# Kernel tuning notes

Hardware: AMD Instinct MI355X
Metric: run time of the kernel (lower is better)

Reference implementation:

```python
import jax, jax.numpy as jnp
import numpy as np


def _lstm_step(x, h, c, Wih, Whh, bih, bhh):
    # PyTorch LSTMCell gate order: i, f, g, o
    g = x @ Wih.T + bih + h @ Whh.T + bhh
    i, f, gg, o = jnp.split(g, 4, axis=1)
    c = jax.nn.sigmoid(f) * c + jax.nn.sigmoid(i) * jnp.tanh(gg)
    h = jax.nn.sigmoid(o) * jnp.tanh(c)
    return h, c


def _canvas2seq(canvas):
    # Valid objects (row-sum >= 0) compacted to the front, rest padded with -1.
    mask = canvas.sum(axis=2) >= 0                       # [B, 25]
    order = jnp.argsort(jnp.where(mask, 0, 1), axis=1, stable=True)
    gathered = jnp.take_along_axis(canvas, order[:, :, None], axis=1)
    smask = jnp.take_along_axis(mask, order, axis=1)
    return jnp.where(smask[:, :, None], gathered, jnp.float32(-1.0))


def _canvas_encode(canvas, Wobj, bobj, ce_Wih, ce_Whh, ce_bih, ce_bhh):
    seq = _canvas2seq(canvas)                            # [B, 25, 4]
    x = seq @ Wobj.T + bobj                              # [B, 25, 64]
    B = x.shape[0]
    h = jnp.zeros((B, 64), x.dtype)
    c = jnp.zeros((B, 64), x.dtype)

    def step(carry, xt):
        h, c = carry
        h, c = _lstm_step(xt, h, c, ce_Wih, ce_Whh, ce_bih, ce_bhh)
        return (h, c), None

    (h, _), _ = jax.lax.scan(step, (h, c), jnp.swapaxes(x, 0, 1))
    return h


def setup_inputs() -> dict:
    key = jax.random.key(0)
    ks = jax.random.split(key, 16)
    B, T, V = 256, 65, 10000
    IN, H = 64, 128
    s = 0.05
    inp = {}
    inp["inst"] = jax.random.randint(ks[0], (B, T), 0, V)
    inp["prev_canvas"] = jax.random.uniform(ks[1], (B, 25, 4), dtype=jnp.float32)
    inp["final_canvas"] = jax.random.uniform(ks[2], (B, 25, 4), dtype=jnp.float32)
    inp["target_obj"] = jax.random.normal(ks[3], (B, 4), dtype=jnp.float32)
    inp["embed_W"] = jax.random.normal(ks[4], (V + 1, IN), dtype=jnp.float32) * s
    inp["Wih"] = jax.random.normal(ks[5], (4 * H, IN), dtype=jnp.float32) * s
    inp["Whh"] = jax.random.normal(ks[6], (4 * H, H), dtype=jnp.float32) * s
    inp["bih"] = jnp.zeros((4 * H,), jnp.float32)
    inp["bhh"] = jnp.zeros((4 * H,), jnp.float32)
    inp["Wout"] = jax.random.normal(ks[7], (V + 1, H), dtype=jnp.float32) * s
    inp["bout"] = jnp.zeros((V + 1,), jnp.float32)
    inp["Wtgt"] = jax.random.normal(ks[8], (IN, 4), dtype=jnp.float32) * s
    inp["btgt"] = jnp.zeros((IN,), jnp.float32)
    inp["Wobj"] = jax.random.normal(ks[9], (64, 4), dtype=jnp.float32) * s
    inp["bobj"] = jnp.zeros((64,), jnp.float32)
    inp["ce_Wih"] = jax.random.normal(ks[10], (256, 64), dtype=jnp.float32) * s
    inp["ce_Whh"] = jax.random.normal(ks[11], (256, 64), dtype=jnp.float32) * s
    inp["ce_bih"] = jnp.zeros((256,), jnp.float32)
    inp["ce_bhh"] = jnp.zeros((256,), jnp.float32)
    return inp


def reference(inst, prev_canvas, final_canvas, target_obj,
              embed_W, Wih, Whh, bih, bhh, Wout, bout,
              Wtgt, btgt, Wobj, bobj, ce_Wih, ce_Whh, ce_bih, ce_bhh):
    B, H = inst.shape[0], 128
    tgt_emb = target_obj @ Wtgt.T + btgt                 # [B, 64]
    enc = (_canvas_encode(prev_canvas, Wobj, bobj, ce_Wih, ce_Whh, ce_bih, ce_bhh)
           + _canvas_encode(final_canvas, Wobj, bobj, ce_Wih, ce_Whh, ce_bih, ce_bhh))
    h = jnp.zeros((B, H), jnp.float32)
    c = jnp.zeros((B, H), jnp.float32)
    h, c = _lstm_step(enc, h, c, Wih, Whh, bih, bhh)
    h, c = _lstm_step(tgt_emb, h, c, Wih, Whh, bih, bhh)

    tokens = inst[:, :-1].T                              # [T-1, B]

    def step(carry, it):
        h, c = carry
        xt = embed_W[it]                                 # [B, 64]
        h, c = _lstm_step(xt, h, c, Wih, Whh, bih, bhh)
        lp = jax.nn.log_softmax(h @ Wout.T + bout, axis=1)
        return (h, c), lp

    _, lps = jax.lax.scan(step, (h, c), tokens)          # [T-1, B, V+1]
    return jnp.swapaxes(lps, 0, 1)                       # [B, T-1, V+1]
```

## Files before the change

kernel.cpp:

```cpp
#include <hip/hip_runtime.h>
#include <stdint.h>

typedef __attribute__((ext_vector_type(4))) float f32x4;
typedef __attribute__((ext_vector_type(8))) short s16x8;
typedef __attribute__((ext_vector_type(8))) unsigned short us8;

__device__ __forceinline__ float bf2f(unsigned short u){
  union { unsigned int i; float f; } v; v.i = ((unsigned int)u) << 16; return v.f;
}
__device__ __forceinline__ unsigned short f2bf(float f){
  union { float f; unsigned int i; } v; v.f = f;
  unsigned int r = v.i + 0x7FFFu + ((v.i >> 16) & 1u);
  return (unsigned short)(r >> 16);
}
__device__ __forceinline__ float sigm(float x){ return 1.0f / (1.0f + __expf(-x)); }

#define NA (10240*128)
#define NB 10240
#define ND 512
#define NE (256*64)
#define NF 32768

__global__ void k_prep(const float* __restrict__ Wout, const float* __restrict__ bout,
                       const float* __restrict__ bih,  const float* __restrict__ bhh,
                       const float* __restrict__ tobj, const float* __restrict__ Wtgt,
                       const float* __restrict__ btgt,
                       const float* __restrict__ ceWih, const float* __restrict__ ceWhh,
                       unsigned short* __restrict__ WoutP, float* __restrict__ boutP,
                       float* __restrict__ bsum, float* __restrict__ tgt,
                       unsigned short* __restrict__ cePack)
{
  int tid = blockIdx.x * 256 + threadIdx.x;
  if (tid < NA){
    int vv = tid >> 7, k = tid & 127;
    float val = (vv < 10001) ? Wout[vv*128 + k] : 0.0f;
    WoutP[tid] = f2bf(val);
  } else if (tid < NA+NB){
    int vv = tid - NA;
    boutP[vv] = (vv < 10001) ? bout[vv] : -1e30f;
  } else if (tid < NA+NB+ND){
    int g = tid - NA - NB;
    bsum[g] = bih[g] + bhh[g];
  } else if (tid < NA+NB+ND+NE){
    int i = tid - NA - NB - ND; int b = i >> 6, j = i & 63;
    const float* to = tobj + b*4; const float* wt = Wtgt + j*4;
    tgt[i] = btgt[j] + to[0]*wt[0] + to[1]*wt[1] + to[2]*wt[2] + to[3]*wt[3];
  } else if (tid < NA+NB+ND+NE+NF){
    int i = tid - NA - NB - ND - NE;
    int half = i >> 14;
    int r = (i >> 6) & 255;
    int k = i & 63;
    int k8 = k >> 3;
    int slot = ((k8 ^ (r & 7)) << 3) | (k & 7);
    const float* src = half ? ceWhh : ceWih;
    cePack[half*16384 + r*64 + slot] = f2bf(src[r*64 + k]);
  }
}

__global__ __launch_bounds__(256) void k_canvas(
    const float* __restrict__ prevC, const float* __restrict__ finC,
    const float* __restrict__ Wobj,  const float* __restrict__ bobj,
    const unsigned short* __restrict__ cePack,
    const float* __restrict__ cebih, const float* __restrict__ cebhh,
    float* __restrict__ encP, float* __restrict__ encF)
{
  __shared__ unsigned short wih[256*64] __attribute__((aligned(16)));
  __shared__ unsigned short whh[256*64] __attribute__((aligned(16)));
  __shared__ float seq[25*4];
  __shared__ float xb[64] __attribute__((aligned(16)));
  __shared__ float hb[2][64] __attribute__((aligned(16)));
  __shared__ float gates[256];
  __shared__ float wobj_s[256];
  __shared__ float bobj_s[64];
  __shared__ float bsum_ce[256];

  int tid = threadIdx.x;
  int b = blockIdx.x & 255;
  int which = blockIdx.x >> 8;
  const float* canvas = (which ? finC : prevC) + b*100;

  {
    const us8* cp = (const us8*)cePack;
    us8* wl = (us8*)wih;
    us8* hl = (us8*)whh;
    for (int i = tid; i < 2048; i += 256){
      wl[i] = cp[i];
      hl[i] = cp[2048 + i];
    }
  }
  wobj_s[tid] = Wobj[tid];
  if (tid < 64) bobj_s[tid] = bobj[tid];
  bsum_ce[tid] = cebih[tid] + cebhh[tid];
  if (tid < 64) hb[0][tid] = 0.0f;
  if (tid == 0){
    int pos = 0;
    for (int i = 0; i < 25; i++){
      float a0=canvas[i*4+0], a1=canvas[i*4+1], a2=canvas[i*4+2], a3=canvas[i*4+3];
      if (a0+a1+a2+a3 >= 0.0f){
        seq[pos*4+0]=a0; seq[pos*4+1]=a1; seq[pos*4+2]=a2; seq[pos*4+3]=a3; pos++;
      }
    }
    for (; pos < 25; pos++){
      seq[pos*4+0]=-1.0f; seq[pos*4+1]=-1.0f; seq[pos*4+2]=-1.0f; seq[pos*4+3]=-1.0f;
    }
  }
  __syncthreads();

  float creg = 0.0f;
  int cur = 0;
  const float4* x4 = (const float4*)xb;

  for (int t = 0; t < 25; t++){
    if (tid < 64){
      float a = bobj_s[tid];
      a += wobj_s[tid*4+0]*seq[t*4+0] + wobj_s[tid*4+1]*seq[t*4+1]
         + wobj_s[tid*4+2]*seq[t*4+2] + wobj_s[tid*4+3]*seq[t*4+3];
      xb[tid] = a;
    }
    __syncthreads();
    float acc = bsum_ce[tid];
    const float4* h4 = (const float4*)hb[cur];
    int rowoff = tid*64;
    int sw = tid & 7;
    #pragma unroll
    for (int k8 = 0; k8 < 8; k8++){
      int slot = ((k8 ^ sw) * 8);
      us8 w1 = *reinterpret_cast<const us8*>(&wih[rowoff + slot]);
      us8 w2 = *reinterpret_cast<const us8*>(&whh[rowoff + slot]);
      float4 xa = x4[2*k8], xc = x4[2*k8+1];
      float4 ha = h4[2*k8], hc = h4[2*k8+1];
      acc += bf2f(w1[0])*xa.x + bf2f(w1[1])*xa.y + bf2f(w1[2])*xa.z + bf2f(w1[3])*xa.w;
      acc += bf2f(w1[4])*xc.x + bf2f(w1[5])*xc.y + bf2f(w1[6])*xc.z + bf2f(w1[7])*xc.w;
      acc += bf2f(w2[0])*ha.x + bf2f(w2[1])*ha.y + bf2f(w2[2])*ha.z + bf2f(w2[3])*ha.w;
      acc += bf2f(w2[4])*hc.x + bf2f(w2[5])*hc.y + bf2f(w2[6])*hc.z + bf2f(w2[7])*hc.w;
    }
    gates[tid] = acc;
    __syncthreads();
    if (tid < 64){
      float i_ = sigm(gates[tid]);
      float f_ = sigm(gates[64+tid]);
      float g_ = tanhf(gates[128+tid]);
      float o_ = sigm(gates[192+tid]);
      creg = f_*creg + i_*g_;
      hb[cur^1][tid] = o_ * tanhf(creg);
    }
    __syncthreads();
    cur ^= 1;
  }
  if (tid < 64){
    (which ? encF : encP)[b*64 + tid] = hb[cur][tid];
  }
}

__global__ __launch_bounds__(512, 2) void k_rec(
    const float* __restrict__ Whh, const float* __restrict__ Wih,
    const float* __restrict__ bsum, const int* __restrict__ inst,
    const float* __restrict__ embW, const float* __restrict__ tgt,
    const float* __restrict__ encP, const float* __restrict__ encF,
    unsigned short* __restrict__ Hout)
{
  int b = blockIdx.x;
  int g = threadIdx.x;
  __shared__ float xb[2][64] __attribute__((aligned(16)));
  __shared__ float hb[2][128] __attribute__((aligned(16)));
  __shared__ float gates[512];

  float wreg[128];
  float ureg[64];
  {
    const float4* wrow = (const float4*)(Whh + g*128);
    #pragma unroll
    for (int k4 = 0; k4 < 32; k4++){
      float4 w = wrow[k4];
      wreg[4*k4+0]=w.x; wreg[4*k4+1]=w.y; wreg[4*k4+2]=w.z; wreg[4*k4+3]=w.w;
    }
    const float4* urow = (const float4*)(Wih + g*64);
    #pragma unroll
    for (int k4 = 0; k4 < 16; k4++){
      float4 w = urow[k4];
      ureg[4*k4+0]=w.x; ureg[4*k4+1]=w.y; ureg[4*k4+2]=w.z; ureg[4*k4+3]=w.w;
    }
  }
  float bz = bsum[g];
  float creg = 0.0f;
  if (g < 128) hb[0][g] = 0.0f;
  if (g < 64)  xb[0][g] = encP[b*64+g] + encF[b*64+g];
  int cur = 0;
  __syncthreads();

  for (int s = 0; s < 66; s++){
    float a0 = bz, a1 = 0.0f, a2 = 0.0f, a3 = 0.0f;
    const float4* h4 = (const float4*)hb[cur];
    const float4* x4 = (const float4*)xb[cur];
    #pragma unroll
    for (int k4 = 0; k4 < 32; k4 += 4){
      float4 h0 = h4[k4], h1 = h4[k4+1], h2 = h4[k4+2], h3 = h4[k4+3];
      a0 += wreg[4*k4+0]*h0.x + wreg[4*k4+1]*h0.y + wreg[4*k4+2]*h0.z + wreg[4*k4+3]*h0.w;
      a1 += wreg[4*k4+4]*h1.x + wreg[4*k4+5]*h1.y + wreg[4*k4+6]*h1.z + wreg[4*k4+7]*h1.w;
      a2 += wreg[4*k4+8]*h2.x + wreg[4*k4+9]*h2.y + wreg[4*k4+10]*h2.z + wreg[4*k4+11]*h2.w;
      a3 += wreg[4*k4+12]*h3.x + wreg[4*k4+13]*h3.y + wreg[4*k4+14]*h3.z + wreg[4*k4+15]*h3.w;
    }
    #pragma unroll
    for (int k4 = 0; k4 < 16; k4 += 4){
      float4 x0 = x4[k4], x1 = x4[k4+1], x2 = x4[k4+2], x3 = x4[k4+3];
      a0 += ureg[4*k4+0]*x0.x + ureg[4*k4+1]*x0.y + ureg[4*k4+2]*x0.z + ureg[4*k4+3]*x0.w;
      a1 += ureg[4*k4+4]*x1.x + ureg[4*k4+5]*x1.y + ureg[4*k4+6]*x1.z + ureg[4*k4+7]*x1.w;
      a2 += ureg[4*k4+8]*x2.x + ureg[4*k4+9]*x2.y + ureg[4*k4+10]*x2.z + ureg[4*k4+11]*x2.w;
      a3 += ureg[4*k4+12]*x3.x + ureg[4*k4+13]*x3.y + ureg[4*k4+14]*x3.z + ureg[4*k4+15]*x3.w;
    }
    gates[g] = (a0 + a1) + (a2 + a3);
    __syncthreads();
    if (g < 128){
      float i_ = sigm(gates[g]);
      float f_ = sigm(gates[128+g]);
      float g_ = tanhf(gates[256+g]);
      float o_ = sigm(gates[384+g]);
      creg = f_*creg + i_*g_;
      float h = o_ * tanhf(creg);
      hb[cur^1][g] = h;
      if (s >= 2) Hout[((size_t)(b*64 + (s-2)))*128 + g] = f2bf(h);
    } else if (g < 192 && s < 65){
      int l = g - 128;
      float v;
      if (s + 1 == 1) v = tgt[b*64 + l];
      else { int tok = inst[b*65 + (s - 1)]; v = embW[tok*64 + l]; }
      xb[cur^1][l] = v;
    }
    __syncthreads();
    cur ^= 1;
  }
}

__global__ __launch_bounds__(512, 4) void k_out(
    const unsigned short* __restrict__ Hout, const unsigned short* __restrict__ WoutP,
    const float* __restrict__ boutP, float* __restrict__ out)
{
  extern __shared__ float stage[];
  __shared__ float rs_l[8][32];
  __shared__ float lse_l[32];

  int blk = blockIdx.x;
  int r0 = blk * 32;
  int tid = threadIdx.x;
  int w = tid >> 6;
  int l = tid & 63;
  int lm = l & 15;
  int lq = l >> 4;
  int kof = lq * 8;
  size_t obase = (size_t)r0 * 10001u;

  s16x8 af[2][4];
  #pragma unroll
  for (int c = 0; c < 2; c++){
    const s16x8* ap = (const s16x8*)(Hout + (size_t)(r0 + c*16 + lm)*128 + kof);
    #pragma unroll
    for (int kk = 0; kk < 4; kk++) af[c][kk] = ap[kk*4];
  }

  s16x8 b0[4], b1[4], b2[4];
#define LOADB(dst, tl) { \
    const s16x8* bp_ = (const s16x8*)(WoutP + (size_t)((tl)*16 + lm)*128 + kof); \
    dst[0] = bp_[0]; dst[1] = bp_[4]; dst[2] = bp_[8]; dst[3] = bp_[12]; }

  float rs[2][4] = {};
#define P1C(buf, tl) { \
    f32x4 a0_ = {0,0,0,0}, a1_ = {0,0,0,0}; \
    _Pragma("unroll") \
    for (int kk = 0; kk < 4; kk++){ \
      a0_ = __builtin_amdgcn_mfma_f32_16x16x32_bf16(af[0][kk], buf[kk], a0_, 0, 0, 0); \
      a1_ = __builtin_amdgcn_mfma_f32_16x16x32_bf16(af[1][kk], buf[kk], a1_, 0, 0, 0); } \
    float bo_ = boutP[(tl)*16 + lm]; \
    _Pragma("unroll") \
    for (int i = 0; i < 4; i++){ rs[0][i] += __expf(a0_[i] + bo_); rs[1][i] += __expf(a1_[i] + bo_); } }

  {
    int tl = w;
    LOADB(b0, tl); LOADB(b1, tl + 8);
    for (int p = 0; p < 26; p++){
      LOADB(b2, tl + 16); P1C(b0, tl);
      LOADB(b0, tl + 24); P1C(b1, tl + 8);
      LOADB(b1, tl + 32); P1C(b2, tl + 16);
      tl += 24;
    }
    P1C(b0, tl);
    P1C(b1, tl + 8);
  }

  #pragma unroll
  for (int c = 0; c < 2; c++){
    #pragma unroll
    for (int i = 0; i < 4; i++){
      float s = rs[c][i];
      s += __shfl_xor(s, 1); s += __shfl_xor(s, 2);
      s += __shfl_xor(s, 4); s += __shfl_xor(s, 8);
      rs[c][i] = s;
    }
  }
  if (lm == 0){
    #pragma unroll
    for (int c = 0; c < 2; c++)
      #pragma unroll
      for (int i = 0; i < 4; i++)
        rs_l[w][c*16 + lq*4 + i] = rs[c][i];
  }

#define T2(c,q) ((c)*32 + w*4 + (q))
  LOADB(b0, T2(0,0)); LOADB(b1, T2(0,1));

#define BAR() { asm volatile("s_waitcnt lgkmcnt(0)" ::: "memory"); __builtin_amdgcn_s_barrier(); }

  BAR();
  if (tid < 32){
    float s = rs_l[0][tid] + rs_l[1][tid] + rs_l[2][tid] + rs_l[3][tid]
            + rs_l[4][tid] + rs_l[5][tid] + rs_l[6][tid] + rs_l[7][tid];
    lse_l[tid] = logf(s);
  }
  BAR();
  float ml[2][4];
  #pragma unroll
  for (int c = 0; c < 2; c++)
    #pragma unroll
    for (int i = 0; i < 4; i++)
      ml[c][i] = lse_l[c*16 + lq*4 + i];

#define P2C(buf, tl, q) { \
    f32x4 a0_ = {0,0,0,0}, a1_ = {0,0,0,0}; \
    _Pragma("unroll") \
    for (int kk = 0; kk < 4; kk++){ \
      a0_ = __builtin_amdgcn_mfma_f32_16x16x32_bf16(af[0][kk], buf[kk], a0_, 0, 0, 0); \
      a1_ = __builtin_amdgcn_mfma_f32_16x16x32_bf16(af[1][kk], buf[kk], a1_, 0, 0, 0); } \
    float bo_ = boutP[(tl)*16 + lm]; \
    int colq_ = (w*4 + (q))*16 + lm; \
    _Pragma("unroll") \
    for (int i = 0; i < 4; i++){ \
      stage[(0*16 + lq*4 + i)*516 + colq_] = a0_[i] + bo_ - ml[0][i]; \
      stage[(1*16 + lq*4 + i)*516 + colq_] = a1_[i] + bo_ - ml[1][i]; } }

#define WPHASE(c) { \
    int vbase_ = (c)*512; \
    if ((c) < 19){ \
      _Pragma("unroll 4") \
      for (int j = 0; j < 32; j++){ \
        int e_ = j*512 + tid; int row_ = e_ >> 9; int cc_ = e_ & 511; \
        __builtin_nontemporal_store(stage[row_*516 + cc_], \
            &out[obase + (size_t)row_*10001u + (unsigned)(vbase_ + cc_)]); } \
    } else { \
      _Pragma("unroll 4") \
      for (int j = 0; j < 32; j++){ \
        int e_ = j*512 + tid; int row_ = e_ >> 9; int cc_ = e_ & 511; \
        if (vbase_ + cc_ < 10001) \
          __builtin_nontemporal_store(stage[row_*516 + cc_], \
              &out[obase + (size_t)row_*10001u + (unsigned)(vbase_ + cc_)]); } } }

#define CHUNK(ba,bb,bc,c) { \
    LOADB(bc, T2(c,2));     P2C(ba, T2(c,0), 0); \
    LOADB(ba, T2(c,3));     P2C(bb, T2(c,1), 1); \
    LOADB(bb, T2((c)+1,0)); P2C(bc, T2(c,2), 2); \
    LOADB(bc, T2((c)+1,1)); P2C(ba, T2(c,3), 3); \
    BAR(); WPHASE(c); BAR(); }

  for (int cb = 0; cb < 18; cb += 3){
    CHUNK(b0, b1, b2, cb);
    CHUNK(b1, b2, b0, cb + 1);
    CHUNK(b2, b0, b1, cb + 2);
  }
  CHUNK(b0, b1, b2, 18);
  LOADB(b0, T2(19,2)); P2C(b1, T2(19,0), 0);
  LOADB(b1, T2(19,3)); P2C(b2, T2(19,1), 1);
  P2C(b0, T2(19,2), 2);
  P2C(b1, T2(19,3), 3);
  BAR();
  WPHASE(19);
}

extern "C" void kernel_launch(void* const* d_in, const int* in_sizes, int n_in,
                              void* d_out, int out_size, void* d_ws, size_t ws_size,
                              hipStream_t stream)
{
  (void)in_sizes; (void)n_in; (void)out_size; (void)ws_size;
  const int*   inst    = (const int*)  d_in[0];
  const float* prevC   = (const float*)d_in[1];
  const float* finC    = (const float*)d_in[2];
  const float* tobj    = (const float*)d_in[3];
  const float* embW    = (const float*)d_in[4];
  const float* Wih     = (const float*)d_in[5];
  const float* Whh     = (const float*)d_in[6];
  const float* bih     = (const float*)d_in[7];
  const float* bhh     = (const float*)d_in[8];
  const float* Wout    = (const float*)d_in[9];
  const float* bout    = (const float*)d_in[10];
  const float* Wtgt    = (const float*)d_in[11];
  const float* btgt    = (const float*)d_in[12];
  const float* Wobj    = (const float*)d_in[13];
  const float* bobj    = (const float*)d_in[14];
  const float* ceWih   = (const float*)d_in[15];
  const float* ceWhh   = (const float*)d_in[16];
  const float* cebih   = (const float*)d_in[17];
  const float* cebhh   = (const float*)d_in[18];

  char* ws = (char*)d_ws;
  unsigned short* WoutP = (unsigned short*)(ws + 0);
  float* boutP = (float*)(ws + 2621440);
  float* bsum  = (float*)(ws + 2662400);
  float* tgt   = (float*)(ws + 2664448);
  float* encP  = (float*)(ws + 2729984);
  float* encF  = (float*)(ws + 2795520);
  unsigned short* Hout = (unsigned short*)(ws + 2861056);
  unsigned short* cePack = (unsigned short*)(ws + 7055360);
  float* out = (float*)d_out;

  hipFuncSetAttribute((const void*)k_out,
                      hipFuncAttributeMaxDynamicSharedMemorySize, 66048);

  k_prep  <<<5354, 256, 0, stream>>>(Wout, bout, bih, bhh, tobj, Wtgt, btgt,
                                     ceWih, ceWhh, WoutP, boutP, bsum, tgt, cePack);
  k_canvas<<<512, 256, 0, stream>>>(prevC, finC, Wobj, bobj, cePack,
                                    cebih, cebhh, encP, encF);
  k_rec   <<<256, 512, 0, stream>>>(Whh, Wih, bsum, inst, embW, tgt, encP, encF, Hout);
  k_out   <<<512, 512, 66048, stream>>>(Hout, WoutP, boutP, out);
}
```

Baseline: 561.6 us.

## Halve rows per block in output projection to raise occupancy

The logits/log-softmax kernel now processes 16 rows per block instead of 32, launches 1024 blocks, and uses static 33KB shared staging with launch bounds allowing 8 waves per SIMD. Register buffers shrink (one A fragment set, double instead of triple B buffering). This aims to improve latency hiding and spread the store-bound work across more resident blocks. In exchange, each block re-reads the full Wout matrix, so Wout traffic doubles and MFMA reuse of each B fragment halves.

```diff
diff --git a/kernel.cpp b/kernel.cpp
--- a/kernel.cpp
+++ b/kernel.cpp
@@ -231,16 +231,16 @@
   }
 }
 
-__global__ __launch_bounds__(512, 4) void k_out(
+__global__ __launch_bounds__(512, 8) void k_out(
     const unsigned short* __restrict__ Hout, const unsigned short* __restrict__ WoutP,
     const float* __restrict__ boutP, float* __restrict__ out)
 {
-  extern __shared__ float stage[];
-  __shared__ float rs_l[8][32];
-  __shared__ float lse_l[32];
+  __shared__ float stage[16*516];
+  __shared__ float rs_l[8][16];
+  __shared__ float lse_l[16];
 
   int blk = blockIdx.x;
-  int r0 = blk * 32;
+  int r0 = blk * 16;
   int tid = threadIdx.x;
   int w = tid >> 6;
   int l = tid & 63;
@@ -249,128 +249,106 @@
   int kof = lq * 8;
   size_t obase = (size_t)r0 * 10001u;
 
-  s16x8 af[2][4];
-  #pragma unroll
-  for (int c = 0; c < 2; c++){
-    const s16x8* ap = (const s16x8*)(Hout + (size_t)(r0 + c*16 + lm)*128 + kof);
-    #pragma unroll
-    for (int kk = 0; kk < 4; kk++) af[c][kk] = ap[kk*4];
-  }
-
-  s16x8 b0[4], b1[4], b2[4];
+  s16x8 af[4];
+  {
+    const s16x8* ap = (const s16x8*)(Hout + (size_t)(r0 + lm)*128 + kof);
+    #pragma unroll
+    for (int kk = 0; kk < 4; kk++) af[kk] = ap[kk*4];
+  }
+
+  s16x8 b0[4], b1[4];
 #define LOADB(dst, tl) { \
     const s16x8* bp_ = (const s16x8*)(WoutP + (size_t)((tl)*16 + lm)*128 + kof); \
     dst[0] = bp_[0]; dst[1] = bp_[4]; dst[2] = bp_[8]; dst[3] = bp_[12]; }
 
-  float rs[2][4] = {};
+  float rs[4] = {0,0,0,0};
 #define P1C(buf, tl) { \
-    f32x4 a0_ = {0,0,0,0}, a1_ = {0,0,0,0}; \
+    f32x4 a_ = {0,0,0,0}; \
     _Pragma("unroll") \
-    for (int kk = 0; kk < 4; kk++){ \
-      a0_ = __builtin_amdgcn_mfma_f32_16x16x32_bf16(af[0][kk], buf[kk], a0_, 0, 0, 0); \
-      a1_ = __builtin_amdgcn_mfma_f32_16x16x32_bf16(af[1][kk], buf[kk], a1_, 0, 0, 0); } \
+    for (int kk = 0; kk < 4; kk++) \
+      a_ = __builtin_amdgcn_mfma_f32_16x16x32_bf16(af[kk], buf[kk], a_, 0, 0, 0); \
     float bo_ = boutP[(tl)*16 + lm]; \
     _Pragma("unroll") \
-    for (int i = 0; i < 4; i++){ rs[0][i] += __expf(a0_[i] + bo_); rs[1][i] += __expf(a1_[i] + bo_); } }
+    for (int i = 0; i < 4; i++) rs[i] += __expf(a_[i] + bo_); }
 
   {
     int tl = w;
-    LOADB(b0, tl); LOADB(b1, tl + 8);
-    for (int p = 0; p < 26; p++){
-      LOADB(b2, tl + 16); P1C(b0, tl);
-      LOADB(b0, tl + 24); P1C(b1, tl + 8);
-      LOADB(b1, tl + 32); P1C(b2, tl + 16);
-      tl += 24;
+    LOADB(b0, tl);
+    for (int p = 0; p < 39; p++){
+      LOADB(b1, tl + 8);  P1C(b0, tl);
+      LOADB(b0, tl + 16); P1C(b1, tl + 8);
+      tl += 16;
     }
     P1C(b0, tl);
+    LOADB(b1, tl + 8);
     P1C(b1, tl + 8);
   }
 
   #pragma unroll
-  for (int c = 0; c < 2; c++){
-    #pragma unroll
-    for (int i = 0; i < 4; i++){
-      float s = rs[c][i];
-      s += __shfl_xor(s, 1); s += __shfl_xor(s, 2);
-      s += __shfl_xor(s, 4); s += __shfl_xor(s, 8);
-      rs[c][i] = s;
-    }
+  for (int i = 0; i < 4; i++){
+    float s = rs[i];
+    s += __shfl_xor(s, 1); s += __shfl_xor(s, 2);
+    s += __shfl_xor(s, 4); s += __shfl_xor(s, 8);
+    rs[i] = s;
   }
   if (lm == 0){
     #pragma unroll
-    for (int c = 0; c < 2; c++)
-      #pragma unroll
-      for (int i = 0; i < 4; i++)
-        rs_l[w][c*16 + lq*4 + i] = rs[c][i];
+    for (int i = 0; i < 4; i++) rs_l[w][lq*4 + i] = rs[i];
   }
 
 #define T2(c,q) ((c)*32 + w*4 + (q))
-  LOADB(b0, T2(0,0)); LOADB(b1, T2(0,1));
+  LOADB(b0, T2(0,0));
 
 #define BAR() { asm volatile("s_waitcnt lgkmcnt(0)" ::: "memory"); __builtin_amdgcn_s_barrier(); }
 
   BAR();
-  if (tid < 32){
+  if (tid < 16){
     float s = rs_l[0][tid] + rs_l[1][tid] + rs_l[2][tid] + rs_l[3][tid]
             + rs_l[4][tid] + rs_l[5][tid] + rs_l[6][tid] + rs_l[7][tid];
     lse_l[tid] = logf(s);
   }
   BAR();
-  float ml[2][4];
+  float ml[4];
   #pragma unroll
-  for (int c = 0; c < 2; c++)
-    #pragma unroll
-    for (int i = 0; i < 4; i++)
-      ml[c][i] = lse_l[c*16 + lq*4 + i];
+  for (int i = 0; i < 4; i++) ml[i] = lse_l[lq*4 + i];
 
 #define P2C(buf, tl, q) { \
-    f32x4 a0_ = {0,0,0,0}, a1_ = {0,0,0,0}; \
+    f32x4 a_ = {0,0,0,0}; \
     _Pragma("unroll") \
-    for (int kk = 0; kk < 4; kk++){ \
-      a0_ = __builtin_amdgcn_mfma_f32_16x16x32_bf16(af[0][kk], buf[kk], a0_, 0, 0, 0); \
-      a1_ = __builtin_amdgcn_mfma_f32_16x16x32_bf16(af[1][kk], buf[kk], a1_, 0, 0, 0); } \
+    for (int kk = 0; kk < 4; kk++) \
+      a_ = __builtin_amdgcn_mfma_f32_16x16x32_bf16(af[kk], buf[kk], a_, 0, 0, 0); \
     float bo_ = boutP[(tl)*16 + lm]; \
     int colq_ = (w*4 + (q))*16 + lm; \
     _Pragma("unroll") \
-    for (int i = 0; i < 4; i++){ \
-      stage[(0*16 + lq*4 + i)*516 + colq_] = a0_[i] + bo_ - ml[0][i]; \
-      stage[(1*16 + lq*4 + i)*516 + colq_] = a1_[i] + bo_ - ml[1][i]; } }
+    for (int i = 0; i < 4; i++) \
+      stage[(lq*4 + i)*516 + colq_] = a_[i] + bo_ - ml[i]; }
 
 #define WPHASE(c) { \
     int vbase_ = (c)*512; \
     if ((c) < 19){ \
       _Pragma("unroll 4") \
-      for (int j = 0; j < 32; j++){ \
+      for (int j = 0; j < 16; j++){ \
         int e_ = j*512 + tid; int row_ = e_ >> 9; int cc_ = e_ & 511; \
         __builtin_nontemporal_store(stage[row_*516 + cc_], \
             &out[obase + (size_t)row_*10001u + (unsigned)(vbase_ + cc_)]); } \
     } else { \
       _Pragma("unroll 4") \
-      for (int j = 0; j < 32; j++){ \
+      for (int j = 0; j < 16; j++){ \
         int e_ = j*512 + tid; int row_ = e_ >> 9; int cc_ = e_ & 511; \
-        if (vbase_ + cc_ < 10001) \
+        if (cc_ < 273) \
           __builtin_nontemporal_store(stage[row_*516 + cc_], \
               &out[obase + (size_t)row_*10001u + (unsigned)(vbase_ + cc_)]); } } }
 
-#define CHUNK(ba,bb,bc,c) { \
-    LOADB(bc, T2(c,2));     P2C(ba, T2(c,0), 0); \
-    LOADB(ba, T2(c,3));     P2C(bb, T2(c,1), 1); \
-    LOADB(bb, T2((c)+1,0)); P2C(bc, T2(c,2), 2); \
-    LOADB(bc, T2((c)+1,1)); P2C(ba, T2(c,3), 3); \
-    BAR(); WPHASE(c); BAR(); }
-
-  for (int cb = 0; cb < 18; cb += 3){
-    CHUNK(b0, b1, b2, cb);
-    CHUNK(b1, b2, b0, cb + 1);
-    CHUNK(b2, b0, b1, cb + 2);
-  }
-  CHUNK(b0, b1, b2, 18);
-  LOADB(b0, T2(19,2)); P2C(b1, T2(19,0), 0);
-  LOADB(b1, T2(19,3)); P2C(b2, T2(19,1), 1);
-  P2C(b0, T2(19,2), 2);
-  P2C(b1, T2(19,3), 3);
-  BAR();
-  WPHASE(19);
+  for (int c = 0; c < 20; c++){
+    LOADB(b1, T2(c,1)); P2C(b0, T2(c,0), 0);
+    LOADB(b0, T2(c,2)); P2C(b1, T2(c,1), 1);
+    LOADB(b1, T2(c,3)); P2C(b0, T2(c,2), 2);
+    if (c < 19) LOADB(b0, T2(c+1,0));
+    P2C(b1, T2(c,3), 3);
+    BAR();
+    WPHASE(c);
+    BAR();
+  }
 }
 
 extern "C" void kernel_launch(void* const* d_in, const int* in_sizes, int n_in,
@@ -409,13 +387,10 @@
   unsigned short* cePack = (unsigned short*)(ws + 7055360);
   float* out = (float*)d_out;
 
-  hipFuncSetAttribute((const void*)k_out,
-                      hipFuncAttributeMaxDynamicSharedMemorySize, 66048);
-
   k_prep  <<<5354, 256, 0, stream>>>(Wout, bout, bih, bhh, tobj, Wtgt, btgt,
                                      ceWih, ceWhh, WoutP, boutP, bsum, tgt, cePack);
   k_canvas<<<512, 256, 0, stream>>>(prevC, finC, Wobj, bobj, cePack,
                                     cebih, cebhh, encP, encF);
   k_rec   <<<256, 512, 0, stream>>>(Whh, Wih, bsum, inst, embW, tgt, encP, encF, Hout);
-  k_out   <<<512, 512, 66048, stream>>>(Hout, WoutP, boutP, out);
-}
+  k_out   <<<1024, 512, 0, stream>>>(Hout, WoutP, boutP, out);
+}
```

After: 978.7 us. 1.74x slower.

## Align output row writes in k_out by staging an extra skew column tile

Applied to the files above, without the earlier changes.

The output projection kernel's write-out phase is restructured so each thread writes one row segment with a per-row skew. The skew makes global stores line up with 16-float boundaries despite the 10001-wide row stride. Wave 0 computes an extra 16-column tile per chunk to cover the shifted range, the stage row pitch grows from 516 to 532, and the triple-buffer chunk schedule becomes a simpler double-buffered loop. The aim is fewer partial or misaligned transactions on the large output write, at the cost of extra MFMA work on one wave, more shared memory, and less overlap of loads.

```diff
diff --git a/kernel.cpp b/kernel.cpp
--- a/kernel.cpp
+++ b/kernel.cpp
@@ -330,47 +330,53 @@
       a0_ = __builtin_amdgcn_mfma_f32_16x16x32_bf16(af[0][kk], buf[kk], a0_, 0, 0, 0); \
       a1_ = __builtin_amdgcn_mfma_f32_16x16x32_bf16(af[1][kk], buf[kk], a1_, 0, 0, 0); } \
     float bo_ = boutP[(tl)*16 + lm]; \
-    int colq_ = (w*4 + (q))*16 + lm; \
+    int colq_ = ((w)*4 + (q))*16 + lm; \
     _Pragma("unroll") \
     for (int i = 0; i < 4; i++){ \
-      stage[(0*16 + lq*4 + i)*516 + colq_] = a0_[i] + bo_ - ml[0][i]; \
-      stage[(1*16 + lq*4 + i)*516 + colq_] = a1_[i] + bo_ - ml[1][i]; } }
+      stage[(0*16 + lq*4 + i)*532 + colq_] = a0_[i] + bo_ - ml[0][i]; \
+      stage[(1*16 + lq*4 + i)*532 + colq_] = a1_[i] + bo_ - ml[1][i]; } }
 
 #define WPHASE(c) { \
-    int vbase_ = (c)*512; \
-    if ((c) < 19){ \
-      _Pragma("unroll 4") \
+    if ((c) == 0){ \
+      _Pragma("unroll") \
       for (int j = 0; j < 32; j++){ \
-        int e_ = j*512 + tid; int row_ = e_ >> 9; int cc_ = e_ & 511; \
-        __builtin_nontemporal_store(stage[row_*516 + cc_], \
-            &out[obase + (size_t)row_*10001u + (unsigned)(vbase_ + cc_)]); } \
+        const int s_ = (16 - (j & 15)) & 15; \
+        __builtin_nontemporal_store(stage[j*532 + tid], \
+            &out[obase + (size_t)j*10001u + (unsigned)tid]); \
+        if (tid < s_) \
+          __builtin_nontemporal_store(stage[j*532 + 512 + tid], \
+              &out[obase + (size_t)j*10001u + (unsigned)(512 + tid)]); \
+      } \
+    } else if ((c) < 19){ \
+      _Pragma("unroll") \
+      for (int j = 0; j < 32; j++){ \
+        const int s_ = (16 - (j & 15)) & 15; \
+        __builtin_nontemporal_store(stage[j*532 + s_ + tid], \
+            &out[obase + (size_t)j*10001u + (unsigned)((c)*512 + s_ + tid)]); \
+      } \
     } else { \
-      _Pragma("unroll 4") \
+      _Pragma("unroll") \
       for (int j = 0; j < 32; j++){ \
-        int e_ = j*512 + tid; int row_ = e_ >> 9; int cc_ = e_ & 511; \
-        if (vbase_ + cc_ < 10001) \
-          __builtin_nontemporal_store(stage[row_*516 + cc_], \
-              &out[obase + (size_t)row_*10001u + (unsigned)(vbase_ + cc_)]); } } }
-
-#define CHUNK(ba,bb,bc,c) { \
-    LOADB(bc, T2(c,2));     P2C(ba, T2(c,0), 0); \
-    LOADB(ba, T2(c,3));     P2C(bb, T2(c,1), 1); \
-    LOADB(bb, T2((c)+1,0)); P2C(bc, T2(c,2), 2); \
-    LOADB(bc, T2((c)+1,1)); P2C(ba, T2(c,3), 3); \
-    BAR(); WPHASE(c); BAR(); }
-
-  for (int cb = 0; cb < 18; cb += 3){
-    CHUNK(b0, b1, b2, cb);
-    CHUNK(b1, b2, b0, cb + 1);
-    CHUNK(b2, b0, b1, cb + 2);
-  }
-  CHUNK(b0, b1, b2, 18);
-  LOADB(b0, T2(19,2)); P2C(b1, T2(19,0), 0);
-  LOADB(b1, T2(19,3)); P2C(b2, T2(19,1), 1);
-  P2C(b0, T2(19,2), 2);
-  P2C(b1, T2(19,3), 3);
-  BAR();
-  WPHASE(19);
+        const int s_ = (16 - (j & 15)) & 15; \
+        if (tid < 273 - s_) \
+          __builtin_nontemporal_store(stage[j*532 + s_ + tid], \
+              &out[obase + (size_t)j*10001u + (unsigned)(19*512 + s_ + tid)]); \
+      } \
+    } }
+
+  for (int c = 0; c < 20; c++){
+    if (w == 0 && c < 19) LOADB(b2, c*32 + 32);
+    LOADB(b1, T2(c,1)); P2C(b0, T2(c,0), 0);
+    LOADB(b0, T2(c,2)); P2C(b1, T2(c,1), 1);
+    LOADB(b1, T2(c,3)); P2C(b0, T2(c,2), 2);
+    if (c < 19) LOADB(b0, T2(c+1,0));
+    P2C(b1, T2(c,3), 3);
+    if (w == 0 && c < 19) P2C(b2, c*32 + 32, 32);
+    if (c < 19) LOADB(b1, T2(c+1,1));
+    BAR();
+    WPHASE(c);
+    BAR();
+  }
 }
 
 extern "C" void kernel_launch(void* const* d_in, const int* in_sizes, int n_in,
@@ -410,12 +416,12 @@
   float* out = (float*)d_out;
 
   hipFuncSetAttribute((const void*)k_out,
-                      hipFuncAttributeMaxDynamicSharedMemorySize, 66048);
+                      hipFuncAttributeMaxDynamicSharedMemorySize, 68096);
 
   k_prep  <<<5354, 256, 0, stream>>>(Wout, bout, bih, bhh, tobj, Wtgt, btgt,
                                      ceWih, ceWhh, WoutP, boutP, bsum, tgt, cePack);
   k_canvas<<<512, 256, 0, stream>>>(prevC, finC, Wobj, bobj, cePack,
                                     cebih, cebhh, encP, encF);
   k_rec   <<<256, 512, 0, stream>>>(Whh, Wih, bsum, inst, embW, tgt, encP, encF, Hout);
-  k_out   <<<512, 512, 66048, stream>>>(Hout, WoutP, boutP, out);
-}
+  k_out   <<<512, 512, 68096, stream>>>(Hout, WoutP, boutP, out);
+}
```

After: 557.1 us. Within noise of the previous version (-0.8%).

## Give each wave a private staging tile to remove block barriers in output phase

Applied to the files above, without the earlier changes.

The output-projection kernel now gives each of the 8 waves its own 32x68 shared-memory staging region. Each wave computes its 64 columns and writes them to global memory itself, so the two block-wide barriers per 512-column chunk are gone. The triple-buffered B-fragment pipeline becomes a simpler double buffer with loads issued between MFMA groups, which may expose more load latency. Each store is now a 64-wide row segment rather than a full 512-wide row, and shared memory per block grows slightly, which could affect occupancy.

```diff
diff --git a/kernel.cpp b/kernel.cpp
--- a/kernel.cpp
+++ b/kernel.cpp
@@ -248,6 +248,7 @@
   int lq = l >> 4;
   int kof = lq * 8;
   size_t obase = (size_t)r0 * 10001u;
+  float* myStage = stage + w * (32*68);
 
   s16x8 af[2][4];
   #pragma unroll
@@ -323,54 +324,42 @@
     for (int i = 0; i < 4; i++)
       ml[c][i] = lse_l[c*16 + lq*4 + i];
 
-#define P2C(buf, tl, q) { \
+#define P2CW(buf, tl, q) { \
     f32x4 a0_ = {0,0,0,0}, a1_ = {0,0,0,0}; \
     _Pragma("unroll") \
     for (int kk = 0; kk < 4; kk++){ \
       a0_ = __builtin_amdgcn_mfma_f32_16x16x32_bf16(af[0][kk], buf[kk], a0_, 0, 0, 0); \
       a1_ = __builtin_amdgcn_mfma_f32_16x16x32_bf16(af[1][kk], buf[kk], a1_, 0, 0, 0); } \
     float bo_ = boutP[(tl)*16 + lm]; \
-    int colq_ = (w*4 + (q))*16 + lm; \
+    int colq_ = (q)*16 + lm; \
     _Pragma("unroll") \
     for (int i = 0; i < 4; i++){ \
-      stage[(0*16 + lq*4 + i)*516 + colq_] = a0_[i] + bo_ - ml[0][i]; \
-      stage[(1*16 + lq*4 + i)*516 + colq_] = a1_[i] + bo_ - ml[1][i]; } }
-
-#define WPHASE(c) { \
-    int vbase_ = (c)*512; \
-    if ((c) < 19){ \
-      _Pragma("unroll 4") \
-      for (int j = 0; j < 32; j++){ \
-        int e_ = j*512 + tid; int row_ = e_ >> 9; int cc_ = e_ & 511; \
-        __builtin_nontemporal_store(stage[row_*516 + cc_], \
-            &out[obase + (size_t)row_*10001u + (unsigned)(vbase_ + cc_)]); } \
-    } else { \
-      _Pragma("unroll 4") \
-      for (int j = 0; j < 32; j++){ \
-        int e_ = j*512 + tid; int row_ = e_ >> 9; int cc_ = e_ & 511; \
-        if (vbase_ + cc_ < 10001) \
-          __builtin_nontemporal_store(stage[row_*516 + cc_], \
-              &out[obase + (size_t)row_*10001u + (unsigned)(vbase_ + cc_)]); } } }
-
-#define CHUNK(ba,bb,bc,c) { \
-    LOADB(bc, T2(c,2));     P2C(ba, T2(c,0), 0); \
-    LOADB(ba, T2(c,3));     P2C(bb, T2(c,1), 1); \
-    LOADB(bb, T2((c)+1,0)); P2C(bc, T2(c,2), 2); \
-    LOADB(bc, T2((c)+1,1)); P2C(ba, T2(c,3), 3); \
-    BAR(); WPHASE(c); BAR(); }
-
-  for (int cb = 0; cb < 18; cb += 3){
-    CHUNK(b0, b1, b2, cb);
-    CHUNK(b1, b2, b0, cb + 1);
-    CHUNK(b2, b0, b1, cb + 2);
-  }
-  CHUNK(b0, b1, b2, 18);
-  LOADB(b0, T2(19,2)); P2C(b1, T2(19,0), 0);
-  LOADB(b1, T2(19,3)); P2C(b2, T2(19,1), 1);
-  P2C(b0, T2(19,2), 2);
-  P2C(b1, T2(19,3), 3);
-  BAR();
-  WPHASE(19);
+      myStage[(0*16 + lq*4 + i)*68 + colq_] = a0_[i] + bo_ - ml[0][i]; \
+      myStage[(1*16 + lq*4 + i)*68 + colq_] = a1_[i] + bo_ - ml[1][i]; } }
+
+  for (int c = 0; c < 20; c++){
+    P2CW(b0, T2(c,0), 0);
+    P2CW(b1, T2(c,1), 1);
+    LOADB(b0, T2(c,2)); LOADB(b1, T2(c,3));
+    P2CW(b0, T2(c,2), 2);
+    P2CW(b1, T2(c,3), 3);
+    if (c < 19){ LOADB(b0, T2(c+1,0)); LOADB(b1, T2(c+1,1)); }
+    asm volatile("s_waitcnt lgkmcnt(0)" ::: "memory");
+    int cbase = c*512 + w*64;
+    int lim = 10001 - cbase;
+    if (lim >= 64){
+      #pragma unroll 4
+      for (int j = 0; j < 32; j++)
+        __builtin_nontemporal_store(myStage[j*68 + l],
+            &out[obase + (size_t)j*10001u + (unsigned)(cbase + l)]);
+    } else if (lim > 0){
+      #pragma unroll 4
+      for (int j = 0; j < 32; j++)
+        if (l < lim)
+          __builtin_nontemporal_store(myStage[j*68 + l],
+              &out[obase + (size_t)j*10001u + (unsigned)(cbase + l)]);
+    }
+  }
 }
 
 extern "C" void kernel_launch(void* const* d_in, const int* in_sizes, int n_in,
@@ -410,12 +399,12 @@
   float* out = (float*)d_out;
 
   hipFuncSetAttribute((const void*)k_out,
-                      hipFuncAttributeMaxDynamicSharedMemorySize, 66048);
+                      hipFuncAttributeMaxDynamicSharedMemorySize, 69632);
 
   k_prep  <<<5354, 256, 0, stream>>>(Wout, bout, bih, bhh, tobj, Wtgt, btgt,
                                      ceWih, ceWhh, WoutP, boutP, bsum, tgt, cePack);
   k_canvas<<<512, 256, 0, stream>>>(prevC, finC, Wobj, bobj, cePack,
                                     cebih, cebhh, encP, encF);
   k_rec   <<<256, 512, 0, stream>>>(Whh, Wih, bsum, inst, embW, tgt, encP, encF, Hout);
-  k_out   <<<512, 512, 66048, stream>>>(Hout, WoutP, boutP, out);
-}
+  k_out   <<<512, 512, 69632, stream>>>(Hout, WoutP, boutP, out);
+}
```

After: 634.5 us. 13.0% more time.
